# Performance work log

Hardware: AMD Instinct MI355X
Metric: run time of the kernel (lower is better)

The kernel has to match this reference:

```python
import jax, jax.numpy as jnp
import numpy as np

B, N, K, D, H, L = 2, 2048, 256, 768, 256, 64
REL_PROP = 3
NUM_BUCKETS = 64


def _pair_scores(u, dist_feat, left_w, left_b, right_w, right_b, out_w, out_b):
    # OptFFpairs-style pairwise scorer: left(u)_i + right(u)_j + dist_emb -> relu -> out
    left = jnp.einsum('bkd,hd->bkh', u, left_w) + left_b    # [B,K,H]
    right = jnp.einsum('bkd,hd->bkh', u, right_w) + right_b  # [B,K,H]
    h = jax.nn.relu(left[:, :, None, :] + right[:, None, :, :] + dist_feat)  # [B,K,K,H]
    return jnp.einsum('bijh,lh->bijl', h, out_w) + out_b     # [B,K,K,L]


def setup_inputs():
    key = jax.random.key(0)
    ks = jax.random.split(key, 12)
    s = 0.02
    all_span_vecs = jax.random.normal(ks[0], (B, N, D), dtype=jnp.float32)
    span_vecs = jax.random.normal(ks[1], (B, K, D), dtype=jnp.float32)
    span_begin = jnp.sort(jax.random.randint(ks[2], (B, K), 0, 1000), axis=-1).astype(jnp.int32)
    span_end = (span_begin + jax.random.randint(ks[3], (B, K), 1, 16)).astype(jnp.int32)
    square_mask = jnp.ones((B, K, K), dtype=jnp.float32)
    span_lengths = jnp.full((B,), float(K), dtype=jnp.float32)
    prune_indices = jnp.stack([
        jnp.sort(jax.random.choice(jax.random.fold_in(ks[4], b), N, (K,), replace=False))
        for b in range(B)
    ]).astype(jnp.int32)
    return {
        'all_span_vecs': all_span_vecs, 'span_vecs': span_vecs,
        'span_begin': span_begin, 'span_end': span_end,
        'square_mask': square_mask, 'span_lengths': span_lengths,
        'prune_indices': prune_indices,
        'left_w': jax.random.normal(ks[5], (H, D)) * s, 'left_b': jnp.zeros((H,), jnp.float32),
        'right_w': jax.random.normal(ks[6], (H, D)) * s, 'right_b': jnp.zeros((H,), jnp.float32),
        'dist_emb': jax.random.normal(ks[7], (NUM_BUCKETS, H)) * s,
        'out_w': jax.random.normal(ks[8], (L, H)) * s, 'out_b': jnp.zeros((L,), jnp.float32),
        'A_w': jax.random.normal(ks[9], (D, L)) * s,
        'B_w': jax.random.normal(ks[10], (D, L)) * s,
        'gate_w': jax.random.normal(ks[11], (D, 2 * D)) * s, 'gate_b': jnp.zeros((D,), jnp.float32),
    }


def reference(all_span_vecs, span_vecs, span_begin, span_end, square_mask, span_lengths,
              prune_indices, left_w, left_b, right_w, right_b, dist_emb, out_w, out_b,
              A_w, B_w, gate_w, gate_b):
    # distance-bucket embedding of the span pair (span_pair_generator)
    dist = span_begin[:, None, :] - span_end[:, :, None]                 # [B,K,K]
    buckets = jnp.clip(jnp.abs(dist), 0, NUM_BUCKETS - 1)
    dist_feat = dist_emb[buckets]                                        # [B,K,K,H]
    inv_len = 1.0 / span_lengths[:, None, None]                          # [B,1,1]

    update = span_vecs
    scores = _pair_scores(update, dist_feat, left_w, left_b, right_w, right_b, out_w, out_b)
    for _ in range(REL_PROP):
        probs = jax.nn.sigmoid(scores) * square_mask[..., None]          # [B,K,K,L]
        # torch: (A(probs) * update.unsqueeze(-2)).sum(-3) -> sum over i (rows)
        ctxt1 = jnp.einsum('bijl,dl,bid->bjd', probs, A_w, update) * inv_len
        # torch: (B(probs) * update.unsqueeze(-3)).sum(-2) -> sum over j (cols)
        ctxt2 = jnp.einsum('bijl,dl,bjd->bid', probs, B_w, update) * inv_len
        c = ctxt1 + ctxt2
        # MyGate: sigmoid-gated convex combination of old state and context
        g = jax.nn.sigmoid(jnp.concatenate([update, c], axis=-1) @ gate_w.T + gate_b)
        update = g * update + (1.0 - g) * c
        scores = _pair_scores(update, dist_feat, left_w, left_b, right_w, right_b, out_w, out_b)

    # overwrite_spans: scatter updated filtered spans back into the full span tensor
    valid = jnp.arange(K)[None, :] < span_lengths[:, None]               # [B,K]
    old = jnp.take_along_axis(all_span_vecs, prune_indices[..., None], axis=1)
    vals = jnp.where(valid[..., None], update, old)
    bidx = jnp.arange(B)[:, None]
    new_all = all_span_vecs.at[bidx, prune_indices].set(vals)
    return new_all, update, scores
```

## Files before the change

kernel.cpp:

```cpp
#include <hip/hip_runtime.h>

#define B_ 2
#define N_ 2048
#define K_ 256
#define D_ 768
#define H_ 256
#define L_ 64
#define BK_ (B_*K_)

typedef __attribute__((ext_vector_type(8))) __bf16 bf16x8;
typedef __attribute__((ext_vector_type(8))) unsigned short ushort8;
typedef __attribute__((ext_vector_type(4))) unsigned short ushort4v;
typedef __attribute__((ext_vector_type(4))) float f32x4;

__device__ __forceinline__ float sigm(float x) { return 1.0f / (1.0f + __expf(-x)); }

__device__ __forceinline__ unsigned short f2b(float f) {
    union { float f; unsigned int u; } v; v.f = f;
    unsigned int u = v.u;
    return (unsigned short)((u + 0x7FFFu + ((u >> 16) & 1u)) >> 16);
}
__device__ __forceinline__ float b2f(unsigned short us) {
    union { unsigned int u; float f; } v; v.u = ((unsigned int)us) << 16;
    return v.f;
}
__device__ __forceinline__ bf16x8 ldb(const unsigned short* p) {
    ushort8 v = *(const ushort8*)p;
    return __builtin_bit_cast(bf16x8, v);
}
__device__ __forceinline__ bf16x8 cvt8(const float* p) {
    float4 v0 = *(const float4*)p;
    float4 v1 = *(const float4*)(p + 4);
    ushort8 u;
    u[0] = f2b(v0.x); u[1] = f2b(v0.y); u[2] = f2b(v0.z); u[3] = f2b(v0.w);
    u[4] = f2b(v1.x); u[5] = f2b(v1.y); u[6] = f2b(v1.z); u[7] = f2b(v1.w);
    return __builtin_bit_cast(bf16x8, u);
}

__global__ __launch_bounds__(256) void conv_all(
    const float* __restrict__ lw, const float* __restrict__ rw,
    const float* __restrict__ ow, const float* __restrict__ gw,
    const float* __restrict__ aw, const float* __restrict__ bw,
    const float* __restrict__ sv, const float* __restrict__ de,
    unsigned short* __restrict__ lwb, unsigned short* __restrict__ rwb,
    unsigned short* __restrict__ owb, unsigned short* __restrict__ gwb,
    unsigned short* __restrict__ wab, unsigned short* __restrict__ wbb,
    unsigned short* __restrict__ ub, unsigned short* __restrict__ deb)
{
    int i4 = (blockIdx.x * 256 + threadIdx.x) * 4;
    const float* src; unsigned short* dst; int off;
    if      (i4 <  196608) { src = lw; dst = lwb; off = 0; }
    else if (i4 <  393216) { src = rw; dst = rwb; off = 196608; }
    else if (i4 <  409600) { src = ow; dst = owb; off = 393216; }
    else if (i4 < 1589248) { src = gw; dst = gwb; off = 409600; }
    else if (i4 < 1638400) { src = aw; dst = wab; off = 1589248; }
    else if (i4 < 1687552) { src = bw; dst = wbb; off = 1638400; }
    else if (i4 < 2080768) { src = sv; dst = ub;  off = 1687552; }
    else if (i4 < 2097152) { src = de; dst = deb; off = 2080768; }
    else return;
    int j = i4 - off;
    float4 v = *(const float4*)&src[j];
    ushort4v p; p.x = f2b(v.x); p.y = f2b(v.y); p.z = f2b(v.z); p.w = f2b(v.w);
    *(ushort4v*)&dst[j] = p;
}

__global__ __launch_bounds__(64) void lr_mfma(
    const unsigned short* __restrict__ Ub,
    const unsigned short* __restrict__ lwb, const float* __restrict__ lb,
    const unsigned short* __restrict__ rwb, const float* __restrict__ rb,
    float* __restrict__ outL, unsigned short* __restrict__ outRb)
{
    const int side = blockIdx.z;
    const unsigned short* __restrict__ W = side ? rwb : lwb;
    const float* __restrict__ bias = side ? rb : lb;
    const int r0 = blockIdx.x * 16, n0 = blockIdx.y * 64;
    const int lane = threadIdx.x;
    const int col = lane & 15, quad = lane >> 4;
    const unsigned short* arow = &Ub[(size_t)(r0 + col)*D_ + quad*8];
    f32x4 acc[4] = {};
    #pragma unroll 4
    for (int kc = 0; kc < D_; kc += 32) {
        bf16x8 a = ldb(arow + kc);
        #pragma unroll
        for (int nt = 0; nt < 4; ++nt) {
            bf16x8 bb = ldb(&W[(size_t)(n0 + nt*16 + col)*D_ + kc + quad*8]);
            acc[nt] = __builtin_amdgcn_mfma_f32_16x16x32_bf16(a, bb, acc[nt], 0, 0, 0);
        }
    }
    #pragma unroll
    for (int nt = 0; nt < 4; ++nt) {
        const int n = n0 + nt*16 + col;
        const float bv = bias[n];
        #pragma unroll
        for (int r = 0; r < 4; ++r) {
            const size_t idx = (size_t)(r0 + quad*4 + r)*H_ + n;
            if (side) outRb[idx] = f2b(acc[nt][r] + bv);
            else      outL[idx] = acc[nt][r] + bv;
        }
    }
}

__global__ __launch_bounds__(256, 1) void scores_v6(
    const float* __restrict__ leftb, const unsigned short* __restrict__ rbb,
    const int* __restrict__ span_begin, const int* __restrict__ span_end,
    const unsigned short* __restrict__ deb, const unsigned short* __restrict__ owb,
    const float* __restrict__ out_b, const float* __restrict__ mask,
    float* __restrict__ S, unsigned short* __restrict__ Pt, int writeP)
{
    const int j0 = blockIdx.x * 64;
    const int i0 = blockIdx.y * 8;
    const int b  = blockIdx.z;
    const int tid = threadIdx.x;
    const int w = tid >> 6, lane = tid & 63, col = lane & 15, quad = lane >> 4;
    const int jrow = w*16 + col;

    __shared__ unsigned short sR[64][264];
    __shared__ float sL[8][256];
    __shared__ float sT[64][68];
    __shared__ float sMask[8][64];
    __shared__ int   sBkt[8][64];

    #pragma unroll
    for (int q = 0; q < 2; ++q) {
        int p = tid + q*256;
        int ii = p >> 6, jj = p & 63;
        int d = span_begin[b*K_ + j0 + jj] - span_end[b*K_ + i0 + ii];
        if (d < 0) d = -d;
        sBkt[ii][jj] = d > 63 ? 63 : d;
        sMask[ii][jj] = mask[(size_t)(b*K_ + i0 + ii)*K_ + j0 + jj];
    }
    #pragma unroll
    for (int q = 0; q < 2; ++q) {
        int f = tid + q*256;
        int row = f >> 6, c4 = (f & 63) * 4;
        *(float4*)&sL[row][c4] = *(const float4*)&leftb[(size_t)(b*K_ + i0 + row)*H_ + c4];
    }
    #pragma unroll
    for (int q = 0; q < 8; ++q) {
        int c = tid + q*256;
        int row = c >> 5, ch = c & 31;
        *(ushort8*)&sR[row][ch*8] = *(const ushort8*)&rbb[(size_t)(b*K_ + j0 + row)*H_ + ch*8];
    }
    bf16x8 bb[4][8];
    #pragma unroll
    for (int lt = 0; lt < 4; ++lt)
        #pragma unroll
        for (int k = 0; k < 8; ++k)
            bb[lt][k] = ldb(&owb[(size_t)(lt*16 + col)*H_ + k*32 + quad*8]);
    float ob[4];
    #pragma unroll
    for (int lt = 0; lt < 4; ++lt) ob[lt] = out_b[lt*16 + col];
    __syncthreads();

    for (int i = 0; i < 8; ++i) {
        const int bkt = sBkt[i][jrow];
        const unsigned short* dr = &deb[(size_t)bkt*H_ + quad*8];
        const float* lrow = &sL[i][quad*8];
        f32x4 acc[4] = {};
        #pragma unroll
        for (int k = 0; k < 8; ++k) {
            float4 l0 = *(const float4*)&lrow[k*32];
            float4 l1 = *(const float4*)&lrow[k*32 + 4];
            ushort8 rv = *(const ushort8*)&sR[jrow][k*32 + quad*8];
            ushort8 dv = *(const ushort8*)&dr[k*32];
            ushort8 pk;
            pk[0] = f2b(fmaxf(0.f, l0.x + b2f(rv[0]) + b2f(dv[0])));
            pk[1] = f2b(fmaxf(0.f, l0.y + b2f(rv[1]) + b2f(dv[1])));
            pk[2] = f2b(fmaxf(0.f, l0.z + b2f(rv[2]) + b2f(dv[2])));
            pk[3] = f2b(fmaxf(0.f, l0.w + b2f(rv[3]) + b2f(dv[3])));
            pk[4] = f2b(fmaxf(0.f, l1.x + b2f(rv[4]) + b2f(dv[4])));
            pk[5] = f2b(fmaxf(0.f, l1.y + b2f(rv[5]) + b2f(dv[5])));
            pk[6] = f2b(fmaxf(0.f, l1.z + b2f(rv[6]) + b2f(dv[6])));
            pk[7] = f2b(fmaxf(0.f, l1.w + b2f(rv[7]) + b2f(dv[7])));
            bf16x8 a = __builtin_bit_cast(bf16x8, pk);
            #pragma unroll
            for (int lt = 0; lt < 4; ++lt)
                acc[lt] = __builtin_amdgcn_mfma_f32_16x16x32_bf16(a, bb[lt][k], acc[lt], 0, 0, 0);
        }
        __syncthreads();
        #pragma unroll
        for (int lt = 0; lt < 4; ++lt)
            #pragma unroll
            for (int r = 0; r < 4; ++r)
                sT[w*16 + quad*4 + r][lt*16 + col] = acc[lt][r] + ob[lt];
        __syncthreads();
        const int jj = tid >> 2, seg = (tid & 3) * 16;
        const int j = j0 + jj, ii = i0 + i;
        if (writeP) {
            const float msk = sMask[i][jj];
            ushort8 o0, o1;
            #pragma unroll
            for (int e = 0; e < 8; ++e) {
                o0[e] = f2b(sigm(sT[jj][seg + e]) * msk);
                o1[e] = f2b(sigm(sT[jj][seg + 8 + e]) * msk);
            }
            unsigned short* dst = &Pt[(((size_t)b*K_ + j)*K_ + ii)*L_ + seg];
            *(ushort8*)&dst[0] = o0;
            *(ushort8*)&dst[8] = o1;
        } else {
            float* dst = &S[(((size_t)b*K_ + ii)*K_ + j)*L_ + seg];
            #pragma unroll
            for (int q2 = 0; q2 < 4; ++q2) {
                float4 v;
                v.x = sT[jj][seg + q2*4 + 0];
                v.y = sT[jj][seg + q2*4 + 1];
                v.z = sT[jj][seg + q2*4 + 2];
                v.w = sT[jj][seg + q2*4 + 3];
                *(float4*)&dst[q2*4] = v;
            }
        }
    }
}

__global__ __launch_bounds__(256) void ctxt_kernel(
    const unsigned short* __restrict__ Pt, const float* __restrict__ U,
    const unsigned short* __restrict__ WAb, const unsigned short* __restrict__ WBb,
    const float* __restrict__ lens, float* __restrict__ cacc)
{
    const int tid = threadIdx.x;
    const int bid = blockIdx.x;
    const int g = bid & 63;
    const int d0 = (bid >> 6) << 6;
    const int m0 = (g & 3) << 6;
    const int z = g >> 2;
    const int b = z >> 3;
    const int mode = (z >> 2) & 1;
    const int t0 = (z & 3) << 6;
    const unsigned short* __restrict__ Wb = mode ? WBb : WAb;

    const int lane = tid & 63, w = tid >> 6;
    const int col = lane & 15, quad = lane >> 4;

    __shared__ unsigned short sP[2][64][72];
    __shared__ float sU[64][68];

    {
        const int row = tid >> 2, cg = (tid & 3) * 16;
        const float* usrc = &U[((size_t)(b*K_ + t0 + row))*D_ + d0 + cg];
        #pragma unroll
        for (int u = 0; u < 4; ++u) {
            float4 v = *(const float4*)&usrc[u*4];
            *(float4*)&sU[row][cg + u*4] = v;
        }
    }
    bf16x8 bw[4][2];
    #pragma unroll
    for (int dt = 0; dt < 4; ++dt)
        #pragma unroll
        for (int kc = 0; kc < 2; ++kc)
            bw[dt][kc] = ldb(&Wb[(size_t)(d0 + dt*16 + col)*L_ + kc*32 + quad*8]);

    f32x4 acc[4] = {};
    const int lrow = tid >> 2, c16 = (tid & 3) * 16;
    const unsigned short* psrc0;
    size_t tstep;
    if (mode) {
        psrc0 = &Pt[(((size_t)b*K_ + t0)*K_ + m0 + lrow)*L_ + c16];
        tstep = (size_t)K_ * L_;
    } else {
        psrc0 = &Pt[(((size_t)b*K_ + m0 + lrow)*K_ + t0)*L_ + c16];
        tstep = (size_t)L_;
    }
    const int arow = w*16 + col;

    ushort8 v0 = *(const ushort8*)&psrc0[0];
    ushort8 v1 = *(const ushort8*)&psrc0[8];
    for (int t = 0; t < 64; ++t) {
        unsigned short (*buf)[72] = sP[t & 1];
        *(ushort8*)&buf[lrow][c16] = v0;
        *(ushort8*)&buf[lrow][c16 + 8] = v1;
        if (t < 63) {
            const unsigned short* src = psrc0 + (size_t)(t + 1) * tstep;
            v0 = *(const ushort8*)&src[0];
            v1 = *(const ushort8*)&src[8];
        }
        __syncthreads();
        bf16x8 a0 = ldb(&buf[arow][quad*8]);
        bf16x8 a1 = ldb(&buf[arow][32 + quad*8]);
        #pragma unroll
        for (int dt = 0; dt < 4; ++dt) {
            f32x4 gacc = {0.f, 0.f, 0.f, 0.f};
            gacc = __builtin_amdgcn_mfma_f32_16x16x32_bf16(a0, bw[dt][0], gacc, 0, 0, 0);
            gacc = __builtin_amdgcn_mfma_f32_16x16x32_bf16(a1, bw[dt][1], gacc, 0, 0, 0);
            const float uu = sU[t][dt*16 + col];
            acc[dt] += gacc * uu;
        }
    }
    const float inv_len = 1.0f / lens[b];
    #pragma unroll
    for (int dt = 0; dt < 4; ++dt)
        #pragma unroll
        for (int r = 0; r < 4; ++r) {
            const int m = m0 + w*16 + quad*4 + r;
            atomicAdd(&cacc[((size_t)(b*K_) + m)*D_ + d0 + dt*16 + col],
                      acc[dt][r] * inv_len);
        }
}

__global__ __launch_bounds__(64) void gate_mfma(
    const unsigned short* __restrict__ Ub, const unsigned short* __restrict__ gwb,
    const float* __restrict__ gb,
    const float* __restrict__ Ucur, const float* __restrict__ Cc,
    float* __restrict__ Unext, unsigned short* __restrict__ Ubnext)
{
    const int r0 = blockIdx.x * 16, n0 = blockIdx.y * 64;
    const int lane = threadIdx.x;
    const int col = lane & 15, quad = lane >> 4;
    const unsigned short* arow_u = &Ub[(size_t)(r0 + col)*D_ + quad*8];
    const float* arow_c = &Cc[(size_t)(r0 + col)*D_ + quad*8];
    f32x4 acc[4] = {};
    #pragma unroll 4
    for (int kc = 0; kc < D_; kc += 32) {
        bf16x8 a = ldb(arow_u + kc);
        #pragma unroll
        for (int nt = 0; nt < 4; ++nt) {
            bf16x8 bb = ldb(&gwb[(size_t)(n0 + nt*16 + col)*(2*D_) + kc + quad*8]);
            acc[nt] = __builtin_amdgcn_mfma_f32_16x16x32_bf16(a, bb, acc[nt], 0, 0, 0);
        }
    }
    #pragma unroll 4
    for (int kc = 0; kc < D_; kc += 32) {
        bf16x8 a = cvt8(arow_c + kc);
        #pragma unroll
        for (int nt = 0; nt < 4; ++nt) {
            bf16x8 bb = ldb(&gwb[(size_t)(n0 + nt*16 + col)*(2*D_) + D_ + kc + quad*8]);
            acc[nt] = __builtin_amdgcn_mfma_f32_16x16x32_bf16(a, bb, acc[nt], 0, 0, 0);
        }
    }
    #pragma unroll
    for (int nt = 0; nt < 4; ++nt) {
        const int n = n0 + nt*16 + col;
        const float gbv = gb[n];
        #pragma unroll
        for (int r = 0; r < 4; ++r) {
            const size_t idx = (size_t)(r0 + quad*4 + r)*D_ + n;
            const float gg = sigm(acc[nt][r] + gbv);
            const float o = gg * Ucur[idx] + (1.f - gg) * Cc[idx];
            Unext[idx] = o;
            Ubnext[idx] = f2b(o);
        }
    }
}

__global__ __launch_bounds__(256) void scatter_kernel(
    const float* __restrict__ upd, const int* __restrict__ prune,
    const float* __restrict__ lens, float* __restrict__ out_all)
{
    const int blk = blockIdx.x;
    const int b = blk / K_, k = blk % K_;
    if ((float)k < lens[b]) {
        const int pi = prune[b*K_ + k];
        const int tid = threadIdx.x;
        if (tid < D_/4) {
            float4 v = *(const float4*)&upd[((size_t)b*K_ + k)*D_ + tid*4];
            *(float4*)&out_all[((size_t)b*N_ + pi)*D_ + tid*4] = v;
        }
    }
}

extern "C" void kernel_launch(void* const* d_in, const int* in_sizes, int n_in,
                              void* d_out, int out_size, void* d_ws, size_t ws_size,
                              hipStream_t stream) {
    (void)in_sizes; (void)n_in; (void)out_size; (void)ws_size;
    const float* all_span_vecs = (const float*)d_in[0];
    const float* span_vecs     = (const float*)d_in[1];
    const int*   span_begin    = (const int*)d_in[2];
    const int*   span_end      = (const int*)d_in[3];
    const float* mask          = (const float*)d_in[4];
    const float* lens          = (const float*)d_in[5];
    const int*   prune         = (const int*)d_in[6];
    const float* lw  = (const float*)d_in[7];
    const float* lb  = (const float*)d_in[8];
    const float* rw  = (const float*)d_in[9];
    const float* rb  = (const float*)d_in[10];
    const float* dist_emb = (const float*)d_in[11];
    const float* out_w    = (const float*)d_in[12];
    const float* out_b    = (const float*)d_in[13];
    const float* A_w = (const float*)d_in[14];
    const float* B_w = (const float*)d_in[15];
    const float* gw  = (const float*)d_in[16];
    const float* gb  = (const float*)d_in[17];

    float* out_all = (float*)d_out;
    float* out_upd = out_all + (size_t)B_*N_*D_;
    float* out_sc  = out_upd + (size_t)BK_*D_;

    float* ws     = (float*)d_ws;
    float* leftb  = ws;
    float* U0     = leftb + (size_t)BK_*H_;
    float* U1     = U0 + (size_t)BK_*D_;
    float* cbuf   = U1 + (size_t)BK_*D_;
    unsigned short* WAb = (unsigned short*)(cbuf + (size_t)BK_*D_);
    unsigned short* WBb = WAb + (size_t)D_*L_;
    unsigned short* lwb = WBb + (size_t)D_*L_;
    unsigned short* rwb = lwb + (size_t)H_*D_;
    unsigned short* owb = rwb + (size_t)H_*D_;
    unsigned short* gwb = owb + (size_t)L_*H_;
    unsigned short* deb = gwb + (size_t)D_*2*D_;
    unsigned short* rbb = deb + (size_t)64*H_;
    unsigned short* Ub0 = rbb + (size_t)BK_*H_;
    unsigned short* Ub1 = Ub0 + (size_t)BK_*D_;
    unsigned short* Pt  = Ub1 + (size_t)BK_*D_;

    hipMemcpyAsync(out_all, all_span_vecs, sizeof(float)*(size_t)B_*N_*D_,
                   hipMemcpyDeviceToDevice, stream);

    dim3 blk256(256), blk64(64);
    conv_all<<<dim3(2048), blk256, 0, stream>>>(lw, rw, out_w, gw, A_w, B_w, span_vecs, dist_emb,
                                                lwb, rwb, owb, gwb, WAb, WBb, Ub0, deb);
    lr_mfma<<<dim3(BK_/16, H_/64, 2), blk64, 0, stream>>>(Ub0, lwb, lb, rwb, rb, leftb, rbb);
    scores_v6<<<dim3(K_/64, K_/8, B_), blk256, 0, stream>>>(leftb, rbb, span_begin, span_end,
                                                            deb, owb, out_b, mask,
                                                            out_sc, Pt, 1);
    const float* Ucur = span_vecs;
    const unsigned short* Ubcur = Ub0;
    float* nexts[3] = {U0, U1, out_upd};
    unsigned short* nextsUb[3] = {Ub1, Ub0, Ub1};
    for (int it = 0; it < 3; ++it) {
        hipMemsetAsync(cbuf, 0, sizeof(float)*(size_t)BK_*D_, stream);
        ctxt_kernel<<<dim3(768), blk256, 0, stream>>>(Pt, Ucur, WAb, WBb, lens, cbuf);
        gate_mfma<<<dim3(BK_/16, D_/64), blk64, 0, stream>>>(Ubcur, gwb, gb,
                                                             Ucur, cbuf, nexts[it], nextsUb[it]);
        Ucur = nexts[it];
        Ubcur = nextsUb[it];
        lr_mfma<<<dim3(BK_/16, H_/64, 2), blk64, 0, stream>>>(Ubcur, lwb, lb, rwb, rb, leftb, rbb);
        scores_v6<<<dim3(K_/64, K_/8, B_), blk256, 0, stream>>>(leftb, rbb, span_begin, span_end,
                                                                deb, owb, out_b, mask,
                                                                out_sc, Pt, it == 2 ? 0 : 1);
    }
    scatter_kernel<<<dim3(BK_), blk256, 0, stream>>>(out_upd, prune, lens, out_all);
}
```

Before: 443.3 us.

## Restructure scores loop order and retile context kernel over full D per block

The scores kernel now computes all 8 rows' MFMA accumulators with k as the outer loop. It reads the right projection and distance embeddings in fp32 straight from global memory instead of staging bf16 copies in shared memory, and uses native bf16 conversion. The context kernel is retiled so each block covers all 768 D columns for 16 rows and streams P and U with a two-stage double buffer. This cuts the grid from 768 to 256 blocks and reuses each P tile across 12 column tiles. The cost is much higher register pressure (acc[8][4] in scores, bw[12][2] and acc[12] in ctxt) and fewer blocks to fill the GPU.

Result: slower. 811.4 us (+83.0%).

```diff
diff --git a/kernel.cpp b/kernel.cpp
--- a/kernel.cpp
+++ b/kernel.cpp
@@ -20,6 +20,10 @@
     unsigned int u = v.u;
     return (unsigned short)((u + 0x7FFFu + ((u >> 16) & 1u)) >> 16);
 }
+__device__ __forceinline__ unsigned short f2bc(float f) {
+    __bf16 h = (__bf16)f;
+    return __builtin_bit_cast(unsigned short, h);
+}
 __device__ __forceinline__ float b2f(unsigned short us) {
     union { unsigned int u; float f; } v; v.u = ((unsigned int)us) << 16;
     return v.f;
@@ -41,11 +45,11 @@
     const float* __restrict__ lw, const float* __restrict__ rw,
     const float* __restrict__ ow, const float* __restrict__ gw,
     const float* __restrict__ aw, const float* __restrict__ bw,
-    const float* __restrict__ sv, const float* __restrict__ de,
+    const float* __restrict__ sv,
     unsigned short* __restrict__ lwb, unsigned short* __restrict__ rwb,
     unsigned short* __restrict__ owb, unsigned short* __restrict__ gwb,
     unsigned short* __restrict__ wab, unsigned short* __restrict__ wbb,
-    unsigned short* __restrict__ ub, unsigned short* __restrict__ deb)
+    unsigned short* __restrict__ ub)
 {
     int i4 = (blockIdx.x * 256 + threadIdx.x) * 4;
     const float* src; unsigned short* dst; int off;
@@ -56,7 +60,6 @@
     else if (i4 < 1638400) { src = aw; dst = wab; off = 1589248; }
     else if (i4 < 1687552) { src = bw; dst = wbb; off = 1638400; }
     else if (i4 < 2080768) { src = sv; dst = ub;  off = 1687552; }
-    else if (i4 < 2097152) { src = de; dst = deb; off = 2080768; }
     else return;
     int j = i4 - off;
     float4 v = *(const float4*)&src[j];
@@ -68,11 +71,12 @@
     const unsigned short* __restrict__ Ub,
     const unsigned short* __restrict__ lwb, const float* __restrict__ lb,
     const unsigned short* __restrict__ rwb, const float* __restrict__ rb,
-    float* __restrict__ outL, unsigned short* __restrict__ outRb)
+    float* __restrict__ outL, float* __restrict__ outR)
 {
     const int side = blockIdx.z;
     const unsigned short* __restrict__ W = side ? rwb : lwb;
     const float* __restrict__ bias = side ? rb : lb;
+    float* __restrict__ outp = side ? outR : outL;
     const int r0 = blockIdx.x * 16, n0 = blockIdx.y * 64;
     const int lane = threadIdx.x;
     const int col = lane & 15, quad = lane >> 4;
@@ -94,16 +98,15 @@
         #pragma unroll
         for (int r = 0; r < 4; ++r) {
             const size_t idx = (size_t)(r0 + quad*4 + r)*H_ + n;
-            if (side) outRb[idx] = f2b(acc[nt][r] + bv);
-            else      outL[idx] = acc[nt][r] + bv;
-        }
-    }
-}
-
-__global__ __launch_bounds__(256, 1) void scores_v6(
-    const float* __restrict__ leftb, const unsigned short* __restrict__ rbb,
+            outp[idx] = acc[nt][r] + bv;
+        }
+    }
+}
+
+__global__ __launch_bounds__(256, 1) void scores_v7(
+    const float* __restrict__ leftb, const float* __restrict__ rightb,
     const int* __restrict__ span_begin, const int* __restrict__ span_end,
-    const unsigned short* __restrict__ deb, const unsigned short* __restrict__ owb,
+    const float* __restrict__ de, const unsigned short* __restrict__ owb,
     const float* __restrict__ out_b, const float* __restrict__ mask,
     float* __restrict__ S, unsigned short* __restrict__ Pt, int writeP)
 {
@@ -114,7 +117,6 @@
     const int w = tid >> 6, lane = tid & 63, col = lane & 15, quad = lane >> 4;
     const int jrow = w*16 + col;
 
-    __shared__ unsigned short sR[64][264];
     __shared__ float sL[8][256];
     __shared__ float sT[64][68];
     __shared__ float sMask[8][64];
@@ -135,54 +137,57 @@
         int row = f >> 6, c4 = (f & 63) * 4;
         *(float4*)&sL[row][c4] = *(const float4*)&leftb[(size_t)(b*K_ + i0 + row)*H_ + c4];
     }
-    #pragma unroll
-    for (int q = 0; q < 8; ++q) {
-        int c = tid + q*256;
-        int row = c >> 5, ch = c & 31;
-        *(ushort8*)&sR[row][ch*8] = *(const ushort8*)&rbb[(size_t)(b*K_ + j0 + row)*H_ + ch*8];
-    }
-    bf16x8 bb[4][8];
-    #pragma unroll
-    for (int lt = 0; lt < 4; ++lt)
-        #pragma unroll
-        for (int k = 0; k < 8; ++k)
-            bb[lt][k] = ldb(&owb[(size_t)(lt*16 + col)*H_ + k*32 + quad*8]);
-    float ob[4];
-    #pragma unroll
-    for (int lt = 0; lt < 4; ++lt) ob[lt] = out_b[lt*16 + col];
     __syncthreads();
 
-    for (int i = 0; i < 8; ++i) {
-        const int bkt = sBkt[i][jrow];
-        const unsigned short* dr = &deb[(size_t)bkt*H_ + quad*8];
-        const float* lrow = &sL[i][quad*8];
-        f32x4 acc[4] = {};
-        #pragma unroll
-        for (int k = 0; k < 8; ++k) {
-            float4 l0 = *(const float4*)&lrow[k*32];
-            float4 l1 = *(const float4*)&lrow[k*32 + 4];
-            ushort8 rv = *(const ushort8*)&sR[jrow][k*32 + quad*8];
-            ushort8 dv = *(const ushort8*)&dr[k*32];
-            ushort8 pk;
-            pk[0] = f2b(fmaxf(0.f, l0.x + b2f(rv[0]) + b2f(dv[0])));
-            pk[1] = f2b(fmaxf(0.f, l0.y + b2f(rv[1]) + b2f(dv[1])));
-            pk[2] = f2b(fmaxf(0.f, l0.z + b2f(rv[2]) + b2f(dv[2])));
-            pk[3] = f2b(fmaxf(0.f, l0.w + b2f(rv[3]) + b2f(dv[3])));
-            pk[4] = f2b(fmaxf(0.f, l1.x + b2f(rv[4]) + b2f(dv[4])));
-            pk[5] = f2b(fmaxf(0.f, l1.y + b2f(rv[5]) + b2f(dv[5])));
-            pk[6] = f2b(fmaxf(0.f, l1.z + b2f(rv[6]) + b2f(dv[6])));
-            pk[7] = f2b(fmaxf(0.f, l1.w + b2f(rv[7]) + b2f(dv[7])));
-            bf16x8 a = __builtin_bit_cast(bf16x8, pk);
+    int deoff[8];
+    #pragma unroll
+    for (int i = 0; i < 8; ++i) deoff[i] = sBkt[i][jrow] * H_;
+
+    const float* rrow = &rightb[(size_t)(b*K_ + j0 + jrow)*H_ + quad*8];
+
+    f32x4 acc[8][4] = {};
+    #pragma unroll
+    for (int k = 0; k < 8; ++k) {
+        const float4 r0 = *(const float4*)&rrow[k*32];
+        const float4 r1 = *(const float4*)&rrow[k*32 + 4];
+        bf16x8 bbk[4];
+        #pragma unroll
+        for (int lt = 0; lt < 4; ++lt)
+            bbk[lt] = ldb(&owb[(size_t)(lt*16 + col)*H_ + k*32 + quad*8]);
+        #pragma unroll
+        for (int i = 0; i < 8; ++i) {
+            const float* dr = &de[deoff[i] + k*32 + quad*8];
+            const float4 d0 = *(const float4*)dr;
+            const float4 d1 = *(const float4*)(dr + 4);
+            const float* lr = &sL[i][k*32 + quad*8];
+            const float4 l0 = *(const float4*)lr;
+            const float4 l1 = *(const float4*)(lr + 4);
+            bf16x8 a;
+            a[0] = (__bf16)fmaxf(0.f, l0.x + r0.x + d0.x);
+            a[1] = (__bf16)fmaxf(0.f, l0.y + r0.y + d0.y);
+            a[2] = (__bf16)fmaxf(0.f, l0.z + r0.z + d0.z);
+            a[3] = (__bf16)fmaxf(0.f, l0.w + r0.w + d0.w);
+            a[4] = (__bf16)fmaxf(0.f, l1.x + r1.x + d1.x);
+            a[5] = (__bf16)fmaxf(0.f, l1.y + r1.y + d1.y);
+            a[6] = (__bf16)fmaxf(0.f, l1.z + r1.z + d1.z);
+            a[7] = (__bf16)fmaxf(0.f, l1.w + r1.w + d1.w);
             #pragma unroll
             for (int lt = 0; lt < 4; ++lt)
-                acc[lt] = __builtin_amdgcn_mfma_f32_16x16x32_bf16(a, bb[lt][k], acc[lt], 0, 0, 0);
-        }
+                acc[i][lt] = __builtin_amdgcn_mfma_f32_16x16x32_bf16(a, bbk[lt], acc[i][lt], 0, 0, 0);
+        }
+    }
+
+    float ob[4];
+    #pragma unroll
+    for (int lt = 0; lt < 4; ++lt) ob[lt] = out_b[lt*16 + col];
+
+    for (int i = 0; i < 8; ++i) {
         __syncthreads();
         #pragma unroll
         for (int lt = 0; lt < 4; ++lt)
             #pragma unroll
             for (int r = 0; r < 4; ++r)
-                sT[w*16 + quad*4 + r][lt*16 + col] = acc[lt][r] + ob[lt];
+                sT[w*16 + quad*4 + r][lt*16 + col] = acc[i][lt][r] + ob[lt];
         __syncthreads();
         const int jj = tid >> 2, seg = (tid & 3) * 16;
         const int j = j0 + jj, ii = i0 + i;
@@ -191,8 +196,8 @@
             ushort8 o0, o1;
             #pragma unroll
             for (int e = 0; e < 8; ++e) {
-                o0[e] = f2b(sigm(sT[jj][seg + e]) * msk);
-                o1[e] = f2b(sigm(sT[jj][seg + 8 + e]) * msk);
+                o0[e] = f2bc(sigm(sT[jj][seg + e]) * msk);
+                o1[e] = f2bc(sigm(sT[jj][seg + 8 + e]) * msk);
             }
             unsigned short* dst = &Pt[(((size_t)b*K_ + j)*K_ + ii)*L_ + seg];
             *(ushort8*)&dst[0] = o0;
@@ -212,87 +217,81 @@
     }
 }
 
-__global__ __launch_bounds__(256) void ctxt_kernel(
+__global__ __launch_bounds__(256) void ctxt_v2(
     const unsigned short* __restrict__ Pt, const float* __restrict__ U,
     const unsigned short* __restrict__ WAb, const unsigned short* __restrict__ WBb,
     const float* __restrict__ lens, float* __restrict__ cacc)
 {
+    const int bid = blockIdx.x;
+    const int m0 = (bid & 15) << 4;
+    const int t0 = ((bid >> 4) & 3) << 6;
+    const int mode = (bid >> 6) & 1;
+    const int b = bid >> 7;
+    const unsigned short* __restrict__ Wb = mode ? WBb : WAb;
     const int tid = threadIdx.x;
-    const int bid = blockIdx.x;
-    const int g = bid & 63;
-    const int d0 = (bid >> 6) << 6;
-    const int m0 = (g & 3) << 6;
-    const int z = g >> 2;
-    const int b = z >> 3;
-    const int mode = (z >> 2) & 1;
-    const int t0 = (z & 3) << 6;
-    const unsigned short* __restrict__ Wb = mode ? WBb : WAb;
-
-    const int lane = tid & 63, w = tid >> 6;
-    const int col = lane & 15, quad = lane >> 4;
-
-    __shared__ unsigned short sP[2][64][72];
-    __shared__ float sU[64][68];
-
-    {
-        const int row = tid >> 2, cg = (tid & 3) * 16;
-        const float* usrc = &U[((size_t)(b*K_ + t0 + row))*D_ + d0 + cg];
-        #pragma unroll
-        for (int u = 0; u < 4; ++u) {
-            float4 v = *(const float4*)&usrc[u*4];
-            *(float4*)&sU[row][cg + u*4] = v;
-        }
-    }
-    bf16x8 bw[4][2];
-    #pragma unroll
-    for (int dt = 0; dt < 4; ++dt)
+    const int w = tid >> 6, lane = tid & 63, col = lane & 15, quad = lane >> 4;
+    const int dbase = w * 192;
+
+    __shared__ unsigned short sP[2][16][72];
+    __shared__ float sU[2][768];
+
+    bf16x8 bw[12][2];
+    #pragma unroll
+    for (int dt = 0; dt < 12; ++dt)
         #pragma unroll
         for (int kc = 0; kc < 2; ++kc)
-            bw[dt][kc] = ldb(&Wb[(size_t)(d0 + dt*16 + col)*L_ + kc*32 + quad*8]);
-
-    f32x4 acc[4] = {};
-    const int lrow = tid >> 2, c16 = (tid & 3) * 16;
-    const unsigned short* psrc0;
-    size_t tstep;
-    if (mode) {
-        psrc0 = &Pt[(((size_t)b*K_ + t0)*K_ + m0 + lrow)*L_ + c16];
-        tstep = (size_t)K_ * L_;
-    } else {
-        psrc0 = &Pt[(((size_t)b*K_ + m0 + lrow)*K_ + t0)*L_ + c16];
-        tstep = (size_t)L_;
-    }
-    const int arow = w*16 + col;
-
-    ushort8 v0 = *(const ushort8*)&psrc0[0];
-    ushort8 v1 = *(const ushort8*)&psrc0[8];
-    for (int t = 0; t < 64; ++t) {
-        unsigned short (*buf)[72] = sP[t & 1];
-        *(ushort8*)&buf[lrow][c16] = v0;
-        *(ushort8*)&buf[lrow][c16 + 8] = v1;
-        if (t < 63) {
-            const unsigned short* src = psrc0 + (size_t)(t + 1) * tstep;
-            v0 = *(const ushort8*)&src[0];
-            v1 = *(const ushort8*)&src[8];
-        }
-        __syncthreads();
-        bf16x8 a0 = ldb(&buf[arow][quad*8]);
-        bf16x8 a1 = ldb(&buf[arow][32 + quad*8]);
-        #pragma unroll
-        for (int dt = 0; dt < 4; ++dt) {
-            f32x4 gacc = {0.f, 0.f, 0.f, 0.f};
-            gacc = __builtin_amdgcn_mfma_f32_16x16x32_bf16(a0, bw[dt][0], gacc, 0, 0, 0);
-            gacc = __builtin_amdgcn_mfma_f32_16x16x32_bf16(a1, bw[dt][1], gacc, 0, 0, 0);
-            const float uu = sU[t][dt*16 + col];
-            acc[dt] += gacc * uu;
-        }
-    }
+            bw[dt][kc] = ldb(&Wb[(size_t)(dbase + dt*16 + col)*L_ + kc*32 + quad*8]);
+
+    const bool doP = tid < 128, doU = tid < 192;
+    const int prow = (tid & 127) >> 3, pseg = (tid & 7) * 8;
+    size_t pbase, tstep;
+    if (mode) { pbase = (((size_t)b*K_ + t0)*K_ + m0 + prow)*L_ + pseg; tstep = (size_t)K_*L_; }
+    else      { pbase = (((size_t)b*K_ + m0 + prow)*K_ + t0)*L_ + pseg; tstep = (size_t)L_; }
+    const size_t ubase = ((size_t)b*K_ + t0)*D_ + (size_t)(doU ? tid : 0)*4;
+
+    ushort8 pv0, pv1; float4 uv0, uv1;
+    if (doP) { pv0 = *(const ushort8*)&Pt[pbase];
+               pv1 = *(const ushort8*)&Pt[pbase + tstep]; }
+    if (doU) { uv0 = *(const float4*)&U[ubase];
+               uv1 = *(const float4*)&U[ubase + D_]; }
+
+    f32x4 acc[12] = {};
+
+    #define CTXT_PHASE(BUFI, PV, UV, TOFF)                                        \
+    {                                                                             \
+        if (doP) *(ushort8*)&sP[BUFI][prow][pseg] = PV;                           \
+        if (doU) *(float4*)&sU[BUFI][tid*4] = UV;                                 \
+        if (t + (TOFF) < 64) {                                                    \
+            if (doP) PV = *(const ushort8*)&Pt[pbase + (size_t)(t + (TOFF))*tstep]; \
+            if (doU) UV = *(const float4*)&U[ubase + (size_t)(t + (TOFF))*D_];    \
+        }                                                                         \
+        __syncthreads();                                                          \
+        bf16x8 a0 = ldb(&sP[BUFI][col][quad*8]);                                  \
+        bf16x8 a1 = ldb(&sP[BUFI][col][32 + quad*8]);                             \
+        _Pragma("unroll")                                                         \
+        for (int dt = 0; dt < 12; ++dt) {                                         \
+            f32x4 g = {0.f, 0.f, 0.f, 0.f};                                       \
+            g = __builtin_amdgcn_mfma_f32_16x16x32_bf16(a0, bw[dt][0], g, 0, 0, 0); \
+            g = __builtin_amdgcn_mfma_f32_16x16x32_bf16(a1, bw[dt][1], g, 0, 0, 0); \
+            const float uu = sU[BUFI][dbase + dt*16 + col];                       \
+            acc[dt] += g * uu;                                                    \
+        }                                                                         \
+        __syncthreads();                                                          \
+    }
+
+    for (int t = 0; t < 64; t += 2) {
+        CTXT_PHASE(0, pv0, uv0, 2)
+        CTXT_PHASE(1, pv1, uv1, 3)
+    }
+    #undef CTXT_PHASE
+
     const float inv_len = 1.0f / lens[b];
     #pragma unroll
-    for (int dt = 0; dt < 4; ++dt)
+    for (int dt = 0; dt < 12; ++dt)
         #pragma unroll
         for (int r = 0; r < 4; ++r) {
-            const int m = m0 + w*16 + quad*4 + r;
-            atomicAdd(&cacc[((size_t)(b*K_) + m)*D_ + d0 + dt*16 + col],
+            const int m = m0 + quad*4 + r;
+            atomicAdd(&cacc[((size_t)(b*K_) + m)*D_ + dbase + dt*16 + col],
                       acc[dt][r] * inv_len);
         }
 }
@@ -387,7 +386,8 @@
 
     float* ws     = (float*)d_ws;
     float* leftb  = ws;
-    float* U0     = leftb + (size_t)BK_*H_;
+    float* rightf = leftb + (size_t)BK_*H_;
+    float* U0     = rightf + (size_t)BK_*H_;
     float* U1     = U0 + (size_t)BK_*D_;
     float* cbuf   = U1 + (size_t)BK_*D_;
     unsigned short* WAb = (unsigned short*)(cbuf + (size_t)BK_*D_);
@@ -396,9 +396,7 @@
     unsigned short* rwb = lwb + (size_t)H_*D_;
     unsigned short* owb = rwb + (size_t)H_*D_;
     unsigned short* gwb = owb + (size_t)L_*H_;
-    unsigned short* deb = gwb + (size_t)D_*2*D_;
-    unsigned short* rbb = deb + (size_t)64*H_;
-    unsigned short* Ub0 = rbb + (size_t)BK_*H_;
+    unsigned short* Ub0 = gwb + (size_t)D_*2*D_;
     unsigned short* Ub1 = Ub0 + (size_t)BK_*D_;
     unsigned short* Pt  = Ub1 + (size_t)BK_*D_;
 
@@ -406,11 +404,11 @@
                    hipMemcpyDeviceToDevice, stream);
 
     dim3 blk256(256), blk64(64);
-    conv_all<<<dim3(2048), blk256, 0, stream>>>(lw, rw, out_w, gw, A_w, B_w, span_vecs, dist_emb,
-                                                lwb, rwb, owb, gwb, WAb, WBb, Ub0, deb);
-    lr_mfma<<<dim3(BK_/16, H_/64, 2), blk64, 0, stream>>>(Ub0, lwb, lb, rwb, rb, leftb, rbb);
-    scores_v6<<<dim3(K_/64, K_/8, B_), blk256, 0, stream>>>(leftb, rbb, span_begin, span_end,
-                                                            deb, owb, out_b, mask,
+    conv_all<<<dim3(2032), blk256, 0, stream>>>(lw, rw, out_w, gw, A_w, B_w, span_vecs,
+                                                lwb, rwb, owb, gwb, WAb, WBb, Ub0);
+    lr_mfma<<<dim3(BK_/16, H_/64, 2), blk64, 0, stream>>>(Ub0, lwb, lb, rwb, rb, leftb, rightf);
+    scores_v7<<<dim3(K_/64, K_/8, B_), blk256, 0, stream>>>(leftb, rightf, span_begin, span_end,
+                                                            dist_emb, owb, out_b, mask,
                                                             out_sc, Pt, 1);
     const float* Ucur = span_vecs;
     const unsigned short* Ubcur = Ub0;
@@ -418,14 +416,14 @@
     unsigned short* nextsUb[3] = {Ub1, Ub0, Ub1};
     for (int it = 0; it < 3; ++it) {
         hipMemsetAsync(cbuf, 0, sizeof(float)*(size_t)BK_*D_, stream);
-        ctxt_kernel<<<dim3(768), blk256, 0, stream>>>(Pt, Ucur, WAb, WBb, lens, cbuf);
+        ctxt_v2<<<dim3(256), blk256, 0, stream>>>(Pt, Ucur, WAb, WBb, lens, cbuf);
         gate_mfma<<<dim3(BK_/16, D_/64), blk64, 0, stream>>>(Ubcur, gwb, gb,
                                                              Ucur, cbuf, nexts[it], nextsUb[it]);
         Ucur = nexts[it];
         Ubcur = nextsUb[it];
-        lr_mfma<<<dim3(BK_/16, H_/64, 2), blk64, 0, stream>>>(Ubcur, lwb, lb, rwb, rb, leftb, rbb);
-        scores_v6<<<dim3(K_/64, K_/8, B_), blk256, 0, stream>>>(leftb, rbb, span_begin, span_end,
-                                                                deb, owb, out_b, mask,
+        lr_mfma<<<dim3(BK_/16, H_/64, 2), blk64, 0, stream>>>(Ubcur, lwb, lb, rwb, rb, leftb, rightf);
+        scores_v7<<<dim3(K_/64, K_/8, B_), blk256, 0, stream>>>(leftb, rightf, span_begin, span_end,
+                                                                dist_emb, owb, out_b, mask,
                                                                 out_sc, Pt, it == 2 ? 0 : 1);
     }
     scatter_kernel<<<dim3(BK_), blk256, 0, stream>>>(out_upd, prune, lens, out_all);
```
